# Optimization experiments

Hardware: AMD Instinct MI355X
Metric: run time of the kernel (lower is better)

Reference implementation:

```python
import jax, jax.numpy as jnp
import numpy as np

B, DIM, SEQ = 8, 256, 16384
K, RED = 3, 3
HID = DIM // RED          # 85
PAD, STRIDE = 1, 1
EPS = 1e-5                # BatchNorm eps (inference-mode BN with running stats)


def setup_inputs() -> dict:
    key = jax.random.key(0)
    ks = jax.random.split(key, 9)
    return {
        "x": jax.random.normal(ks[0], (B, DIM, SEQ), jnp.float32),
        "w1": jax.random.normal(ks[1], (HID, DIM), jnp.float32) * 0.05,
        "bn_gamma": jax.random.uniform(ks[2], (HID,), jnp.float32, 0.5, 1.5),
        "bn_beta": jax.random.normal(ks[3], (HID,), jnp.float32) * 0.1,
        "bn_mean": jax.random.normal(ks[4], (HID,), jnp.float32) * 0.1,
        "bn_var": jax.random.uniform(ks[5], (HID,), jnp.float32, 0.5, 1.5),
        "w2": jax.random.normal(ks[6], (DIM * K, HID), jnp.float32) * 0.05,
        "b2": jax.random.normal(ks[7], (DIM * K,), jnp.float32) * 0.05,
        "bias": jax.random.normal(ks[8], (DIM,), jnp.float32) * 0.05,
    }


def reference(x, w1, bn_gamma, bn_beta, bn_mean, bn_var, w2, b2, bias):
    b = x.shape[0]
    seq = x.shape[2]
    # squeeze: adaptive avg pool over seq -> [B, DIM]
    pooled = x.mean(axis=2)
    # conv1 (1x1, no bias) + inference BatchNorm + ReLU
    y = jnp.einsum('bc,hc->bh', pooled, w1)
    y = (y - bn_mean) * (bn_gamma * jax.lax.rsqrt(bn_var + EPS)) + bn_beta
    y = jax.nn.relu(y)
    # conv2 (1x1) -> per-sample depthwise kernels [B, DIM, K]
    w = (jnp.einsum('bh,oh->bo', y, w2) + b2).reshape(b, DIM, K)
    # dynamic depthwise conv1d (emulates F.conv1d with groups = B*DIM)
    xp = jnp.pad(x, ((0, 0), (0, 0), (PAD, PAD)))
    out_len = (seq + 2 * PAD - K) // STRIDE + 1
    out = jnp.zeros((b, DIM, out_len), x.dtype)
    for kk in range(K):  # small fixed kernel loop
        out = out + w[:, :, kk:kk + 1] * xp[:, :, kk:kk + out_len * STRIDE:STRIDE]
    return out + bias[None, :, None]
```

## Files before the change

kernel.cpp:

```cpp
#include <hip/hip_runtime.h>

#define B_      8
#define DIM_    256
#define SEQ_    16384
#define K_      3
#define HID_    85
#define OUTCH_  (DIM_ * K_)
#define EPS_    1e-5f

__global__ __launch_bounds__(256) void pool_kernel(const float* __restrict__ x,
                                                   float* __restrict__ pooled) {
    const int row = blockIdx.x;
    const float4* x4 = (const float4*)(x + (size_t)row * SEQ_);
    float s = 0.f;
#pragma unroll
    for (int k = 0; k < SEQ_ / 4 / 256; ++k) {
        float4 v = x4[threadIdx.x + k * 256];
        s += (v.x + v.y) + (v.z + v.w);
    }
#pragma unroll
    for (int off = 32; off > 0; off >>= 1) s += __shfl_down(s, off, 64);
    __shared__ float lds[4];
    const int lane = threadIdx.x & 63, wid = threadIdx.x >> 6;
    if (lane == 0) lds[wid] = s;
    __syncthreads();
    if (threadIdx.x == 0) {
        float t = (lds[0] + lds[1]) + (lds[2] + lds[3]);
        pooled[row] = t * (1.0f / SEQ_);
    }
}

__global__ __launch_bounds__(256) void mlp_kernel(const float* __restrict__ pooled,
                                                  const float* __restrict__ w1,
                                                  const float* __restrict__ gamma,
                                                  const float* __restrict__ beta,
                                                  const float* __restrict__ mean,
                                                  const float* __restrict__ var,
                                                  const float* __restrict__ w2,
                                                  const float* __restrict__ b2,
                                                  float* __restrict__ wout) {
    const int b = blockIdx.x;
    __shared__ float sp[DIM_];
    __shared__ float sy[HID_];
    sp[threadIdx.x] = pooled[b * DIM_ + threadIdx.x];
    __syncthreads();
    if (threadIdx.x < HID_) {
        const int h = threadIdx.x;
        const float* w1r = w1 + h * DIM_;
        float acc = 0.f;
#pragma unroll 8
        for (int c = 0; c < DIM_; ++c) acc = fmaf(sp[c], w1r[c], acc);
        float t = (acc - mean[h]) * (gamma[h] * rsqrtf(var[h] + EPS_)) + beta[h];
        sy[h] = fmaxf(t, 0.f);
    }
    __syncthreads();
    for (int o = threadIdx.x; o < OUTCH_; o += 256) {
        const float* w2r = w2 + o * HID_;
        float acc = b2[o];
        for (int h = 0; h < HID_; ++h) acc = fmaf(sy[h], w2r[h], acc);
        wout[b * OUTCH_ + o] = acc;
    }
}

__global__ __launch_bounds__(256) void conv_kernel(const float* __restrict__ x,
                                                   const float* __restrict__ wk,
                                                   const float* __restrict__ bias,
                                                   float* __restrict__ out) {
    const int row = blockIdx.x;
    const int c = row & (DIM_ - 1);
    const float w0 = wk[row * 3 + 0];
    const float w1 = wk[row * 3 + 1];
    const float w2 = wk[row * 3 + 2];
    const float bs = bias[c];
    const float* xr = x + (size_t)row * SEQ_;
    const float4* x4 = (const float4*)xr;
    float4* o4 = (float4*)(out + (size_t)row * SEQ_);
#pragma unroll
    for (int k = 0; k < SEQ_ / 4 / 256; ++k) {
        const int j = threadIdx.x + k * 256;
        const int s0 = j * 4;
        float4 v = x4[j];
        float left  = (s0 > 0)          ? xr[s0 - 1] : 0.f;
        float right = (s0 + 4 < SEQ_)   ? xr[s0 + 4] : 0.f;
        float4 r;
        r.x = fmaf(w0, left, fmaf(w1, v.x, w2 * v.y)) + bs;
        r.y = fmaf(w0, v.x,  fmaf(w1, v.y, w2 * v.z)) + bs;
        r.z = fmaf(w0, v.y,  fmaf(w1, v.z, w2 * v.w)) + bs;
        r.w = fmaf(w0, v.z,  fmaf(w1, v.w, w2 * right)) + bs;
        o4[j] = r;
    }
}

extern "C" void kernel_launch(void* const* d_in, const int* in_sizes, int n_in,
                              void* d_out, int out_size, void* d_ws, size_t ws_size,
                              hipStream_t stream) {
    const float* x     = (const float*)d_in[0];
    const float* w1    = (const float*)d_in[1];
    const float* gamma = (const float*)d_in[2];
    const float* beta  = (const float*)d_in[3];
    const float* mean  = (const float*)d_in[4];
    const float* var   = (const float*)d_in[5];
    const float* w2    = (const float*)d_in[6];
    const float* b2    = (const float*)d_in[7];
    const float* bias  = (const float*)d_in[8];
    float* out = (float*)d_out;

    float* pooled = (float*)d_ws;
    float* wk     = pooled + B_ * DIM_;

    pool_kernel<<<B_ * DIM_, 256, 0, stream>>>(x, pooled);
    mlp_kernel<<<B_, 256, 0, stream>>>(pooled, w1, gamma, beta, mean, var, w2, b2, wk);
    conv_kernel<<<B_ * DIM_, 256, 0, stream>>>(x, wk, bias, out);
}
```

Before: 298.0 us.

## Fuse MLP into conv kernel, use lane shuffles for halo, nontemporal stores

```diff
diff --git a/kernel.cpp b/kernel.cpp
--- a/kernel.cpp
+++ b/kernel.cpp
@@ -8,14 +8,16 @@
 #define OUTCH_  (DIM_ * K_)
 #define EPS_    1e-5f
 
+typedef float floatx4 __attribute__((ext_vector_type(4)));
+
 __global__ __launch_bounds__(256) void pool_kernel(const float* __restrict__ x,
                                                    float* __restrict__ pooled) {
     const int row = blockIdx.x;
-    const float4* x4 = (const float4*)(x + (size_t)row * SEQ_);
+    const floatx4* x4 = (const floatx4*)(x + (size_t)row * SEQ_);
     float s = 0.f;
 #pragma unroll
     for (int k = 0; k < SEQ_ / 4 / 256; ++k) {
-        float4 v = x4[threadIdx.x + k * 256];
+        floatx4 v = x4[threadIdx.x + k * 256];
         s += (v.x + v.y) + (v.z + v.w);
     }
 #pragma unroll
@@ -30,16 +32,21 @@
     }
 }
 
-__global__ __launch_bounds__(256) void mlp_kernel(const float* __restrict__ pooled,
-                                                  const float* __restrict__ w1,
-                                                  const float* __restrict__ gamma,
-                                                  const float* __restrict__ beta,
-                                                  const float* __restrict__ mean,
-                                                  const float* __restrict__ var,
-                                                  const float* __restrict__ w2,
-                                                  const float* __restrict__ b2,
-                                                  float* __restrict__ wout) {
-    const int b = blockIdx.x;
+__global__ __launch_bounds__(256) void conv_kernel(const float* __restrict__ x,
+                                                   const float* __restrict__ pooled,
+                                                   const float* __restrict__ w1,
+                                                   const float* __restrict__ gamma,
+                                                   const float* __restrict__ beta,
+                                                   const float* __restrict__ mean,
+                                                   const float* __restrict__ var,
+                                                   const float* __restrict__ w2,
+                                                   const float* __restrict__ b2,
+                                                   const float* __restrict__ bias,
+                                                   float* __restrict__ out) {
+    const int row = blockIdx.x;
+    const int b = row >> 8;
+    const int c = row & (DIM_ - 1);
+
     __shared__ float sp[DIM_];
     __shared__ float sy[HID_];
     sp[threadIdx.x] = pooled[b * DIM_ + threadIdx.x];
@@ -49,45 +56,43 @@
         const float* w1r = w1 + h * DIM_;
         float acc = 0.f;
 #pragma unroll 8
-        for (int c = 0; c < DIM_; ++c) acc = fmaf(sp[c], w1r[c], acc);
+        for (int cc = 0; cc < DIM_; ++cc) acc = fmaf(sp[cc], w1r[cc], acc);
         float t = (acc - mean[h]) * (gamma[h] * rsqrtf(var[h] + EPS_)) + beta[h];
         sy[h] = fmaxf(t, 0.f);
     }
     __syncthreads();
-    for (int o = threadIdx.x; o < OUTCH_; o += 256) {
-        const float* w2r = w2 + o * HID_;
-        float acc = b2[o];
-        for (int h = 0; h < HID_; ++h) acc = fmaf(sy[h], w2r[h], acc);
-        wout[b * OUTCH_ + o] = acc;
+
+    const float* w2r0 = w2 + (c * 3 + 0) * HID_;
+    const float* w2r1 = w2 + (c * 3 + 1) * HID_;
+    const float* w2r2 = w2 + (c * 3 + 2) * HID_;
+    float w0 = b2[c * 3 + 0], w1t = b2[c * 3 + 1], w2t = b2[c * 3 + 2];
+    for (int h = 0; h < HID_; ++h) {
+        const float yv = sy[h];
+        w0  = fmaf(yv, w2r0[h], w0);
+        w1t = fmaf(yv, w2r1[h], w1t);
+        w2t = fmaf(yv, w2r2[h], w2t);
     }
-}
+    const float bs = bias[c];
 
-__global__ __launch_bounds__(256) void conv_kernel(const float* __restrict__ x,
-                                                   const float* __restrict__ wk,
-                                                   const float* __restrict__ bias,
-                                                   float* __restrict__ out) {
-    const int row = blockIdx.x;
-    const int c = row & (DIM_ - 1);
-    const float w0 = wk[row * 3 + 0];
-    const float w1 = wk[row * 3 + 1];
-    const float w2 = wk[row * 3 + 2];
-    const float bs = bias[c];
     const float* xr = x + (size_t)row * SEQ_;
-    const float4* x4 = (const float4*)xr;
-    float4* o4 = (float4*)(out + (size_t)row * SEQ_);
+    const floatx4* x4 = (const floatx4*)xr;
+    floatx4* o4 = (floatx4*)(out + (size_t)row * SEQ_);
+    const int lane = threadIdx.x & 63;
 #pragma unroll
     for (int k = 0; k < SEQ_ / 4 / 256; ++k) {
         const int j = threadIdx.x + k * 256;
         const int s0 = j * 4;
-        float4 v = x4[j];
-        float left  = (s0 > 0)          ? xr[s0 - 1] : 0.f;
-        float right = (s0 + 4 < SEQ_)   ? xr[s0 + 4] : 0.f;
-        float4 r;
-        r.x = fmaf(w0, left, fmaf(w1, v.x, w2 * v.y)) + bs;
-        r.y = fmaf(w0, v.x,  fmaf(w1, v.y, w2 * v.z)) + bs;
-        r.z = fmaf(w0, v.y,  fmaf(w1, v.z, w2 * v.w)) + bs;
-        r.w = fmaf(w0, v.z,  fmaf(w1, v.w, w2 * right)) + bs;
-        o4[j] = r;
+        floatx4 v = x4[j];
+        float left  = __shfl_up(v.w, 1, 64);
+        float right = __shfl_down(v.x, 1, 64);
+        if (lane == 0)  left  = (s0 > 0)        ? xr[s0 - 1] : 0.f;
+        if (lane == 63) right = (s0 + 4 < SEQ_) ? xr[s0 + 4] : 0.f;
+        floatx4 r;
+        r.x = fmaf(w0, left, fmaf(w1t, v.x, w2t * v.y)) + bs;
+        r.y = fmaf(w0, v.x,  fmaf(w1t, v.y, w2t * v.z)) + bs;
+        r.z = fmaf(w0, v.y,  fmaf(w1t, v.z, w2t * v.w)) + bs;
+        r.w = fmaf(w0, v.z,  fmaf(w1t, v.w, w2t * right)) + bs;
+        __builtin_nontemporal_store(r, &o4[j]);
     }
 }
 
@@ -106,9 +111,8 @@
     float* out = (float*)d_out;
 
     float* pooled = (float*)d_ws;
-    float* wk     = pooled + B_ * DIM_;
 
     pool_kernel<<<B_ * DIM_, 256, 0, stream>>>(x, pooled);
-    mlp_kernel<<<B_, 256, 0, stream>>>(pooled, w1, gamma, beta, mean, var, w2, b2, wk);
-    conv_kernel<<<B_ * DIM_, 256, 0, stream>>>(x, wk, bias, out);
+    conv_kernel<<<B_ * DIM_, 256, 0, stream>>>(x, pooled, w1, gamma, beta, mean,
+                                               var, w2, b2, bias, out);
 }
```

Result: faster. 292.1 us (-2.0%).
